# Kernel optimization log

Hardware: AMD Instinct MI355X
Metric: run time of the kernel (lower is better)

Reference implementation:

```python
import jax, jax.numpy as jnp
import numpy as np

T, H, NH, NKV, HD = 2048, 1024, 16, 4, 64
I, E, TOPK = 2048, 8, 2
EPS = 1e-5
ROPE_BASE = 10000.0


def rms_norm(x, w):
    var = jnp.mean(x * x, axis=-1, keepdims=True)
    return x * jax.lax.rsqrt(var + EPS) * w


def apply_rope(x, positions, n_heads):
    # neox-style rotary over full head_dim
    t = x.reshape(-1, n_heads, HD)
    half = HD // 2
    inv_freq = 1.0 / (ROPE_BASE ** (jnp.arange(0, half, dtype=jnp.float32) / half))
    freqs = positions.astype(jnp.float32)[:, None] * inv_freq[None, :]  # [T, half]
    cos = jnp.cos(freqs)[:, None, :]
    sin = jnp.sin(freqs)[:, None, :]
    x1, x2 = t[..., :half], t[..., half:]
    rot = jnp.concatenate([x1 * cos - x2 * sin, x2 * cos + x1 * sin], axis=-1)
    return rot.reshape(x.shape)


def setup_inputs():
    key = jax.random.key(0)
    ks = jax.random.split(key, 9)
    s = 0.02
    return dict(
        positions=jnp.arange(T, dtype=jnp.int32),
        hidden_states=jax.random.normal(ks[0], (T, H), jnp.float32),
        input_ln_w=jnp.ones((H,), jnp.float32),
        post_ln_w=jnp.ones((H,), jnp.float32),
        residual_ln_w=jnp.ones((H,), jnp.float32),
        qkv_w=jax.random.normal(ks[1], ((NH + 2 * NKV) * HD, H), jnp.float32) * s,
        o_w=jax.random.normal(ks[2], (H, NH * HD), jnp.float32) * s,
        gate_w=jax.random.normal(ks[3], (E, H), jnp.float32) * s,
        ws=jax.random.normal(ks[4], (E, 2 * I, H), jnp.float32) * s,
        w2s=jax.random.normal(ks[5], (E, H, I), jnp.float32) * s,
        res_w13=jax.random.normal(ks[6], (2 * H, H), jnp.float32) * s,
        res_w2=jax.random.normal(ks[7], (H, H), jnp.float32) * s,
    )


def attention(x, positions, qkv_w, o_w):
    qkv = x @ qkv_w.T  # [T, (NH+2*NKV)*HD]
    q, k, v = jnp.split(qkv, [NH * HD, NH * HD + NKV * HD], axis=-1)
    q = apply_rope(q, positions, NH)
    k = apply_rope(k, positions, NKV)
    q = q.reshape(T, NH, HD)
    k = k.reshape(T, NKV, HD)
    v = v.reshape(T, NKV, HD)
    rep = NH // NKV  # GQA: repeat kv heads
    k = jnp.repeat(k, rep, axis=1)
    v = jnp.repeat(v, rep, axis=1)
    scale = HD ** -0.5
    scores = jnp.einsum('tnd,snd->nts', q, k) * scale  # [NH, T, T]
    causal = jnp.tril(jnp.ones((T, T), dtype=bool))
    scores = jnp.where(causal[None], scores, -jnp.inf)
    probs = jax.nn.softmax(scores, axis=-1)
    out = jnp.einsum('nts,snd->tnd', probs, v).reshape(T, NH * HD)
    return out @ o_w.T


def silu_and_mul(gu):
    g, u = jnp.split(gu, 2, axis=-1)
    return jax.nn.silu(g) * u


def moe(x, gate_w, ws, w2s):
    logits = x @ gate_w.T  # [T, E]
    probs = jax.nn.softmax(logits, axis=-1)
    topk_w, topk_ids = jax.lax.top_k(probs, TOPK)
    topk_w = topk_w / jnp.sum(topk_w, axis=-1, keepdims=True)  # renormalize (top_k > 1)
    routes = jnp.zeros((x.shape[0], E), x.dtype).at[
        jnp.arange(x.shape[0])[:, None], topk_ids].set(topk_w)  # [T, E] sparse routing
    gu = jnp.einsum('th,eih->tei', x, ws)        # [T, E, 2I]
    act = silu_and_mul(gu)                        # [T, E, I]
    eo = jnp.einsum('tei,ehi->teh', act, w2s)     # [T, E, H]
    return jnp.einsum('te,teh->th', routes, eo)


def reference(positions, hidden_states, input_ln_w, post_ln_w, residual_ln_w,
              qkv_w, o_w, gate_w, ws, w2s, res_w13, res_w2):
    residual_input = hidden_states
    h = rms_norm(hidden_states, input_ln_w)
    h = attention(h, positions, qkv_w, o_w)
    residual_attn = residual_input + h
    # parallel residual MLP branch (ffn_dim == hidden)
    r = rms_norm(residual_attn, residual_ln_w)
    r = silu_and_mul(r @ res_w13.T) @ res_w2.T
    residual_mlp = residual_attn + r
    # MoE branch
    m = rms_norm(residual_attn, post_ln_w)
    m = moe(m, gate_w, ws, w2s)
    return residual_mlp + m
```

## Files before the change

kernel.cpp:

```cpp
#include <hip/hip_runtime.h>
#include <stdint.h>


typedef _Float16 f16;
typedef _Float16 f16x8 __attribute__((ext_vector_type(8)));
typedef _Float16 f16x4 __attribute__((ext_vector_type(4)));
typedef float f32x4 __attribute__((ext_vector_type(4)));

#define DEV __device__ __forceinline__

DEV void glds16(const void* g, void* l) {
  __builtin_amdgcn_global_load_lds((const __attribute__((address_space(1))) void*)g,
                                   (__attribute__((address_space(3))) void*)l, 16, 0, 0);
}

__global__ void cvt_f16_kernel(const float* __restrict__ in, f16* __restrict__ outp) {
  const size_t i = ((size_t)blockIdx.x * 256 + threadIdx.x) * 4;
  float4 f = *(const float4*)(in + i);
  f16x4 o;
  o[0] = (f16)f.x; o[1] = (f16)f.y; o[2] = (f16)f.z; o[3] = (f16)f.w;
  *(f16x4*)(outp + i) = o;
}

__global__ void cvt_f16x2_kernel(const float* __restrict__ in,
                                 f16* __restrict__ oh, f16* __restrict__ ol) {
  const size_t i = ((size_t)blockIdx.x * 256 + threadIdx.x) * 4;
  float4 f = *(const float4*)(in + i);
  f16x4 h, l;
  h[0] = (f16)f.x; l[0] = (f16)(f.x - (float)h[0]);
  h[1] = (f16)f.y; l[1] = (f16)(f.y - (float)h[1]);
  h[2] = (f16)f.z; l[2] = (f16)(f.z - (float)h[2]);
  h[3] = (f16)f.w; l[3] = (f16)(f.w - (float)h[3]);
  *(f16x4*)(oh + i) = h;
  *(f16x4*)(ol + i) = l;
}

__global__ void rmsnorm_kernel(const float* __restrict__ in, const float* __restrict__ w,
                               f16* __restrict__ outp) {
  const int t = blockIdx.x * 4 + (threadIdx.x >> 6);
  const int lane = threadIdx.x & 63;
  const float* x = in + (size_t)t * 1024;
  float v[16]; float ss = 0.f;
#pragma unroll
  for (int j = 0; j < 16; j++) { float a = x[lane + 64 * j]; v[j] = a; ss += a * a; }
#pragma unroll
  for (int m = 1; m < 64; m <<= 1) ss += __shfl_xor(ss, m);
  const float rs = rsqrtf(ss * (1.f / 1024.f) + 1e-5f);
#pragma unroll
  for (int j = 0; j < 16; j++)
    outp[(size_t)t * 1024 + lane + 64 * j] = (f16)(v[j] * rs * w[lane + 64 * j]);
}

__global__ void rmsnorm_dual_kernel(const float* __restrict__ in,
                                    const float* __restrict__ w1, const float* __restrict__ w2,
                                    f16* __restrict__ o1, f16* __restrict__ o2) {
  const int t = blockIdx.x * 4 + (threadIdx.x >> 6);
  const int lane = threadIdx.x & 63;
  const float* x = in + (size_t)t * 1024;
  float v[16]; float ss = 0.f;
#pragma unroll
  for (int j = 0; j < 16; j++) { float a = x[lane + 64 * j]; v[j] = a; ss += a * a; }
#pragma unroll
  for (int m = 1; m < 64; m <<= 1) ss += __shfl_xor(ss, m);
  const float rs = rsqrtf(ss * (1.f / 1024.f) + 1e-5f);
#pragma unroll
  for (int j = 0; j < 16; j++) {
    float nv = v[j] * rs;
    size_t idx = (size_t)t * 1024 + lane + 64 * j;
    o1[idx] = (f16)(nv * w1[lane + 64 * j]);
    o2[idx] = (f16)(nv * w2[lane + 64 * j]);
  }
}

template <int EPI, int BN>
__global__ __launch_bounds__(256) void gemm_f16_kernel(
    const f16* __restrict__ A, const f16* __restrict__ B,
    void* __restrict__ outp, const float* __restrict__ addsrc,
    int M, int N, int K) {
  constexpr int JT = BN / 32;
  __shared__ __attribute__((aligned(16))) f16 As[128 * 32];
  __shared__ __attribute__((aligned(16))) f16 Bs[BN * 32];
  const int tid = threadIdx.x;
  const size_t row0 = (size_t)blockIdx.y * 128, col0 = (size_t)blockIdx.x * BN;
  const int c0 = tid, c1 = tid + 256;
  const f16* a0 = A + (row0 + (c0 >> 2)) * K + (c0 & 3) * 8;
  const f16* a1 = A + (row0 + (c1 >> 2)) * K + (c1 & 3) * 8;
  const f16* b0 = B + (col0 + (c0 >> 2)) * K + (c0 & 3) * 8;
  const f16* b1 = B + (col0 + ((BN == 128) ? (c1 >> 2) : 0)) * K + (c1 & 3) * 8;

  const int wave = tid >> 6, lane = tid & 63, lr = lane >> 4, lc = lane & 15;
  const int wr = wave >> 1, wc = wave & 1;

  f32x4 acc[4][JT];
#pragma unroll
  for (int i = 0; i < 4; i++)
#pragma unroll
    for (int j = 0; j < JT; j++) acc[i][j] = (f32x4){0.f, 0.f, 0.f, 0.f};

  for (int k0 = 0; k0 < K; k0 += 32) {
    glds16(a0 + k0, As + c0 * 8); glds16(a1 + k0, As + c1 * 8);
    glds16(b0 + k0, Bs + c0 * 8);
    if constexpr (BN == 128) glds16(b1 + k0, Bs + c1 * 8);
    __syncthreads();
    f16x8 af[4], bfr[JT];
#pragma unroll
    for (int i = 0; i < 4; i++)
      af[i] = *(const f16x8*)(As + (wr * 64 + i * 16 + lc) * 32 + lr * 8);
#pragma unroll
    for (int j = 0; j < JT; j++)
      bfr[j] = *(const f16x8*)(Bs + (wc * (BN / 2) + j * 16 + lc) * 32 + lr * 8);
#pragma unroll
    for (int i = 0; i < 4; i++)
#pragma unroll
      for (int j = 0; j < JT; j++)
        acc[i][j] = __builtin_amdgcn_mfma_f32_16x16x32_f16(af[i], bfr[j], acc[i][j], 0, 0, 0);
    __syncthreads();
  }

#pragma unroll
  for (int i = 0; i < 4; i++)
#pragma unroll
    for (int j = 0; j < JT; j++) {
      const size_t rbase = row0 + wr * 64 + i * 16 + lr * 4;
      const size_t col = col0 + wc * (BN / 2) + j * 16 + lc;
#pragma unroll
      for (int r = 0; r < 4; r++) {
        size_t idx = (rbase + r) * N + col;
        if constexpr (EPI == 0) ((float*)outp)[idx] = acc[i][j][r];
        else if constexpr (EPI == 1) ((float*)outp)[idx] = acc[i][j][r] + addsrc[idx];
        else ((f16*)outp)[idx] = (f16)acc[i][j][r];
      }
    }
}

__global__ __launch_bounds__(256) void gemm_f16x2_add_kernel(
    const f16* __restrict__ Ah, const f16* __restrict__ Al,
    const f16* __restrict__ Bh, const f16* __restrict__ Bl,
    float* __restrict__ outp, const float* __restrict__ addsrc,
    int M, int N, int K) {
  __shared__ __attribute__((aligned(16))) f16 Ash[128 * 32];
  __shared__ __attribute__((aligned(16))) f16 Asl[128 * 32];
  __shared__ __attribute__((aligned(16))) f16 Bsh[64 * 32];
  __shared__ __attribute__((aligned(16))) f16 Bsl[64 * 32];
  const int tid = threadIdx.x;
  const size_t row0 = (size_t)blockIdx.y * 128, col0 = (size_t)blockIdx.x * 64;
  const int c0 = tid, c1 = tid + 256;
  const size_t aoff0 = (row0 + (c0 >> 2)) * K + (c0 & 3) * 8;
  const size_t aoff1 = (row0 + (c1 >> 2)) * K + (c1 & 3) * 8;
  const size_t boff0 = (col0 + (c0 >> 2)) * K + (c0 & 3) * 8;

  const int wave = tid >> 6, lane = tid & 63, lr = lane >> 4, lc = lane & 15;
  const int wr = wave >> 1, wc = wave & 1;

  f32x4 acc[4][2];
#pragma unroll
  for (int i = 0; i < 4; i++)
#pragma unroll
    for (int j = 0; j < 2; j++) acc[i][j] = (f32x4){0.f, 0.f, 0.f, 0.f};

  for (int k0 = 0; k0 < K; k0 += 32) {
    glds16(Ah + aoff0 + k0, Ash + c0 * 8); glds16(Ah + aoff1 + k0, Ash + c1 * 8);
    glds16(Al + aoff0 + k0, Asl + c0 * 8); glds16(Al + aoff1 + k0, Asl + c1 * 8);
    glds16(Bh + boff0 + k0, Bsh + c0 * 8);
    glds16(Bl + boff0 + k0, Bsl + c0 * 8);
    __syncthreads();
    f16x8 afh[4], afl[4], bfh[2], bfl[2];
#pragma unroll
    for (int i = 0; i < 4; i++) {
      const int ro = (wr * 64 + i * 16 + lc) * 32 + lr * 8;
      afh[i] = *(const f16x8*)(Ash + ro);
      afl[i] = *(const f16x8*)(Asl + ro);
    }
#pragma unroll
    for (int j = 0; j < 2; j++) {
      const int ro = (wc * 32 + j * 16 + lc) * 32 + lr * 8;
      bfh[j] = *(const f16x8*)(Bsh + ro);
      bfl[j] = *(const f16x8*)(Bsl + ro);
    }
#pragma unroll
    for (int i = 0; i < 4; i++)
#pragma unroll
      for (int j = 0; j < 2; j++) {
        acc[i][j] = __builtin_amdgcn_mfma_f32_16x16x32_f16(afh[i], bfh[j], acc[i][j], 0, 0, 0);
        acc[i][j] = __builtin_amdgcn_mfma_f32_16x16x32_f16(afh[i], bfl[j], acc[i][j], 0, 0, 0);
        acc[i][j] = __builtin_amdgcn_mfma_f32_16x16x32_f16(afl[i], bfh[j], acc[i][j], 0, 0, 0);
      }
    __syncthreads();
  }

#pragma unroll
  for (int i = 0; i < 4; i++)
#pragma unroll
    for (int j = 0; j < 2; j++) {
      const size_t rbase = row0 + wr * 64 + i * 16 + lr * 4;
      const size_t col = col0 + wc * 32 + j * 16 + lc;
#pragma unroll
      for (int r = 0; r < 4; r++) {
        size_t idx = (rbase + r) * N + col;
        outp[idx] = acc[i][j][r] + addsrc[idx];
      }
    }
}

template <int DIVROW, int BN>
__global__ __launch_bounds__(256) void gemm_moe_kernel(
    const f16* __restrict__ A, const f16* __restrict__ Ball, f16* __restrict__ outp,
    const int* __restrict__ perm, const int* __restrict__ counts,
    int N, int K, size_t strideB) {
  constexpr int JT = BN / 32;
  const int e = blockIdx.z;
  const int cnt = counts[e];
  const int bm = blockIdx.y;
  if (bm * 128 >= cnt) return;
  const f16* B = Ball + (size_t)e * strideB;
  __shared__ __attribute__((aligned(16))) f16 As[128 * 32];
  __shared__ __attribute__((aligned(16))) f16 Bs[BN * 32];
  const int tid = threadIdx.x;
  const size_t col0 = (size_t)blockIdx.x * BN;
  const int c0 = tid, c1 = tid + 256;
  const int pbase = e * 2048 + bm * 128;
  const int rt0 = c0 >> 2, rt1 = c1 >> 2;
  const int sid0 = (bm * 128 + rt0 < cnt) ? perm[pbase + rt0] : -1;
  const int sid1 = (bm * 128 + rt1 < cnt) ? perm[pbase + rt1] : -1;
  const size_t ar0 = DIVROW ? (size_t)(sid0 >> 1) : (size_t)sid0;
  const size_t ar1 = DIVROW ? (size_t)(sid1 >> 1) : (size_t)sid1;
  const f16* ap0 = A + ar0 * K + (c0 & 3) * 8;
  const f16* ap1 = A + ar1 * K + (c1 & 3) * 8;
  const f16* b0 = B + (col0 + (c0 >> 2)) * K + (c0 & 3) * 8;
  const f16* b1 = B + (col0 + ((BN == 128) ? (c1 >> 2) : 0)) * K + (c1 & 3) * 8;

  const int wave = tid >> 6, lane = tid & 63, lr = lane >> 4, lc = lane & 15;
  const int wr = wave >> 1, wc = wave & 1;

  f32x4 acc[4][JT];
#pragma unroll
  for (int i = 0; i < 4; i++)
#pragma unroll
    for (int j = 0; j < JT; j++) acc[i][j] = (f32x4){0.f, 0.f, 0.f, 0.f};

  for (int k0 = 0; k0 < K; k0 += 32) {
    glds16(b0 + k0, Bs + c0 * 8);
    if constexpr (BN == 128) glds16(b1 + k0, Bs + c1 * 8);
    f16x8 va0, va1;
#pragma unroll
    for (int x = 0; x < 8; x++) { va0[x] = (f16)0.f; va1[x] = (f16)0.f; }
    if (sid0 >= 0) va0 = *(const f16x8*)(ap0 + k0);
    if (sid1 >= 0) va1 = *(const f16x8*)(ap1 + k0);
    *(f16x8*)(As + c0 * 8) = va0;
    *(f16x8*)(As + c1 * 8) = va1;
    __syncthreads();
    f16x8 af[4], bfr[JT];
#pragma unroll
    for (int i = 0; i < 4; i++)
      af[i] = *(const f16x8*)(As + (wr * 64 + i * 16 + lc) * 32 + lr * 8);
#pragma unroll
    for (int j = 0; j < JT; j++)
      bfr[j] = *(const f16x8*)(Bs + (wc * (BN / 2) + j * 16 + lc) * 32 + lr * 8);
#pragma unroll
    for (int i = 0; i < 4; i++)
#pragma unroll
      for (int j = 0; j < JT; j++)
        acc[i][j] = __builtin_amdgcn_mfma_f32_16x16x32_f16(af[i], bfr[j], acc[i][j], 0, 0, 0);
    __syncthreads();
  }

  int sids[4][4];
#pragma unroll
  for (int i = 0; i < 4; i++)
#pragma unroll
    for (int r = 0; r < 4; r++) {
      int rit = wr * 64 + i * 16 + lr * 4 + r;
      sids[i][r] = (bm * 128 + rit < cnt) ? perm[pbase + rit] : -1;
    }
#pragma unroll
  for (int i = 0; i < 4; i++)
#pragma unroll
    for (int j = 0; j < JT; j++) {
      const size_t col = col0 + wc * (BN / 2) + j * 16 + lc;
#pragma unroll
      for (int r = 0; r < 4; r++)
        if (sids[i][r] >= 0)
          outp[(size_t)sids[i][r] * N + col] = (f16)acc[i][j][r];
    }
}

__global__ void rope_kernel(const float* __restrict__ qkv, const int* __restrict__ pos,
                            f16* __restrict__ qr, f16* __restrict__ kr) {
  const int t = blockIdx.y;
  const int u = blockIdx.x * 256 + threadIdx.x;
  if (u >= 640) return;
  const float* base = qkv + (size_t)t * 1536;
  const int head = u >> 5, i = u & 31;
  const bool isq = head < 16;
  const int off = isq ? head * 64 + i : 1024 + (head - 16) * 64 + i;
  const float x1 = base[off], x2 = base[off + 32];
  const double ph = (double)pos[t] * exp((double)i * -0.28782313662425575);
  const float c = (float)cos(ph), s = (float)sin(ph);
  const float r1 = x1 * c - x2 * s, r2 = x2 * c + x1 * s;
  if (isq) {
    const float qs = 0.18033688011116042f;
    qr[(size_t)t * 1024 + head * 64 + i] = (f16)(qs * r1);
    qr[(size_t)t * 1024 + head * 64 + i + 32] = (f16)(qs * r2);
  } else {
    const int kh = head - 16;
    kr[(size_t)t * 256 + kh * 64 + i] = (f16)r1;
    kr[(size_t)t * 256 + kh * 64 + i + 32] = (f16)r2;
  }
}

__global__ void vtrans_kernel(const float* __restrict__ qkvf, f16* __restrict__ vt) {
  __shared__ float Ts[64 * 69];
  const int t0 = blockIdx.x * 64;
  const int kv = blockIdx.y;
  const int tid = threadIdx.x;
  const int tr = tid >> 2, jj = tid & 3;
  const float* src = qkvf + (size_t)(t0 + tr) * 1536 + 1280 + kv * 64 + jj * 16;
#pragma unroll
  for (int x = 0; x < 4; x++) {
    float4 f = *(const float4*)(src + x * 4);
    Ts[tr * 69 + jj * 16 + x * 4 + 0] = f.x;
    Ts[tr * 69 + jj * 16 + x * 4 + 1] = f.y;
    Ts[tr * 69 + jj * 16 + x * 4 + 2] = f.z;
    Ts[tr * 69 + jj * 16 + x * 4 + 3] = f.w;
  }
  __syncthreads();
  f16* dst = vt + (size_t)(kv * 64 + tr) * 2048 + t0 + jj * 16;
#pragma unroll
  for (int x = 0; x < 2; x++) {
    f16x8 o;
#pragma unroll
    for (int i = 0; i < 8; i++) o[i] = (f16)Ts[(jj * 16 + x * 8 + i) * 69 + tr];
    *(f16x8*)(dst + x * 8) = o;
  }
}

__global__ __launch_bounds__(256, 3) void attn_kernel(
    const f16* __restrict__ qr, const f16* __restrict__ kr, const f16* __restrict__ vt,
    f16* __restrict__ ahi, f16* __restrict__ alo) {
  const int qt = 31 - (int)blockIdx.x;
  const int h = blockIdx.y;
  const int kvh = h >> 2;
  __shared__ __attribute__((aligned(16))) f16 Ks[128 * 72];
  __shared__ __attribute__((aligned(16))) f16 Vs[64 * 136];
  __shared__ __attribute__((aligned(16))) f16 Pl[4 * 16 * 136];
  const int tid = threadIdx.x;
  const int wave = tid >> 6, lane = tid & 63, lr = lane >> 4, lc = lane & 15;
  const int trow = qt * 64 + wave * 16 + lc;
  f16* Pw = Pl + wave * 16 * 136;

  const int krow = tid >> 3, kcol = (tid & 7) * 8;
  const int vrow = tid >> 4, vcol = (tid & 15) * 8;
  const f16* kgbase = kr + (size_t)kvh * 64 + kcol;
  const f16* vgbase = vt + (size_t)(kvh * 64 + vrow) * 2048 + vcol;

  const f16* qp = qr + (size_t)trow * 1024 + h * 64 + lr * 8;
  f16x8 qf0 = *(const f16x8*)(qp);
  f16x8 qf1 = *(const f16x8*)(qp + 32);

  float m_run = -3e38f, l_run = 0.f;
  f32x4 accO[4];
#pragma unroll
  for (int jo = 0; jo < 4; jo++) accO[jo] = (f32x4){0.f, 0.f, 0.f, 0.f};

  const int nch = (qt >> 1) + 1;

  f16x8 kreg[4], vreg[4];
#pragma unroll
  for (int it = 0; it < 4; it++) {
    kreg[it] = *(const f16x8*)(kgbase + (size_t)(it * 32 + krow) * 256);
    vreg[it] = *(const f16x8*)(vgbase + it * 16 * 2048);
  }

  for (int ch = 0; ch < nch; ++ch) {
    const int c0 = ch * 128;
    const bool last = (ch == nch - 1);

    __syncthreads();
#pragma unroll
    for (int it = 0; it < 4; it++) {
      *(f16x8*)(Ks + (it * 32 + krow) * 72 + kcol) = kreg[it];
      *(f16x8*)(Vs + (it * 16 + vrow) * 136 + vcol) = vreg[it];
    }
    __syncthreads();

    if (!last) {
      const int c1 = c0 + 128;
#pragma unroll
      for (int it = 0; it < 4; it++) {
        kreg[it] = *(const f16x8*)(kgbase + (size_t)(c1 + it * 32 + krow) * 256);
        vreg[it] = *(const f16x8*)(vgbase + it * 16 * 2048 + c1);
      }
    }

    f32x4 st[8];
#pragma unroll
    for (int j = 0; j < 8; j++) {
      const f16* kp = Ks + (j * 16 + lc) * 72 + lr * 8;
      f16x8 ka0 = *(const f16x8*)(kp);
      f16x8 ka1 = *(const f16x8*)(kp + 32);
      f32x4 s = (f32x4){0.f, 0.f, 0.f, 0.f};
      s = __builtin_amdgcn_mfma_f32_16x16x32_f16(ka0, qf0, s, 0, 0, 0);
      s = __builtin_amdgcn_mfma_f32_16x16x32_f16(ka1, qf1, s, 0, 0, 0);
      st[j] = s;
    }

    if (last) {
#pragma unroll
      for (int j = 0; j < 8; j++)
#pragma unroll
        for (int r = 0; r < 4; r++)
          if (c0 + j * 16 + lr * 4 + r > trow) st[j][r] = -3e38f;
    }

    float mc = -3e38f;
#pragma unroll
    for (int j = 0; j < 8; j++)
      mc = fmaxf(mc, fmaxf(fmaxf(st[j][0], st[j][1]), fmaxf(st[j][2], st[j][3])));
    mc = fmaxf(mc, __shfl_xor(mc, 16));
    mc = fmaxf(mc, __shfl_xor(mc, 32));
    const float mn = fmaxf(m_run, mc);
    const float alpha = __builtin_amdgcn_exp2f(m_run - mn);
    m_run = mn;

    float ls = 0.f;
#pragma unroll
    for (int j = 0; j < 8; j++) {
      f16x4 pv;
#pragma unroll
      for (int r = 0; r < 4; r++) {
        float e = __builtin_amdgcn_exp2f(st[j][r] - mn);
        ls += e;
        pv[r] = (f16)e;
      }
      *(f16x4*)(Pw + lc * 136 + j * 16 + lr * 4) = pv;
    }
    ls += __shfl_xor(ls, 16);
    ls += __shfl_xor(ls, 32);
    l_run = l_run * alpha + ls;
#pragma unroll
    for (int jo = 0; jo < 4; jo++) accO[jo] *= alpha;

#pragma unroll
    for (int kkt = 0; kkt < 4; kkt++) {
      f16x8 pb = *(const f16x8*)(Pw + lc * 136 + kkt * 32 + lr * 8);
#pragma unroll
      for (int jo = 0; jo < 4; jo++) {
        f16x8 va = *(const f16x8*)(Vs + (jo * 16 + lc) * 136 + kkt * 32 + lr * 8);
        accO[jo] = __builtin_amdgcn_mfma_f32_16x16x32_f16(va, pb, accO[jo], 0, 0, 0);
      }
    }
  }

  const float inv = 1.f / l_run;
#pragma unroll
  for (int jo = 0; jo < 4; jo++) {
    f16x4 hi4, lo4;
#pragma unroll
    for (int r = 0; r < 4; r++) {
      float o = accO[jo][r] * inv;
      f16 hv = (f16)o;
      hi4[r] = hv;
      lo4[r] = (f16)(o - (float)hv);
    }
    const size_t idx = (size_t)trow * 1024 + h * 64 + jo * 16 + lr * 4;
    *(f16x4*)(ahi + idx) = hi4;
    *(f16x4*)(alo + idx) = lo4;
  }
}

__global__ void routing_kernel(const float* __restrict__ resA,
                               const float* __restrict__ postw,
                               const float* __restrict__ gw,
                               int* __restrict__ counts, int* __restrict__ perm,
                               float* __restrict__ rw) {
  const int t = blockIdx.x * 4 + (threadIdx.x >> 6);
  const int lane = threadIdx.x & 63;
  const float* x = resA + (size_t)t * 1024;
  float v[16]; float ss = 0.f;
#pragma unroll
  for (int j = 0; j < 16; j++) { float a = x[lane + 64 * j]; v[j] = a; ss += a * a; }
#pragma unroll
  for (int m = 1; m < 64; m <<= 1) ss += __shfl_xor(ss, m);
  const float rs = rsqrtf(ss * (1.f / 1024.f) + 1e-5f);
#pragma unroll
  for (int j = 0; j < 16; j++) v[j] *= rs * postw[lane + 64 * j];
  float lg[8];
#pragma unroll
  for (int e = 0; e < 8; e++) {
    float p = 0.f;
    const float* g = gw + (size_t)e * 1024;
#pragma unroll
    for (int j = 0; j < 16; j++) p += v[j] * g[lane + 64 * j];
#pragma unroll
    for (int m = 1; m < 64; m <<= 1) p += __shfl_xor(p, m);
    lg[e] = p;
  }
  if (lane == 0) {
    int e0 = 0; float b0 = lg[0];
#pragma unroll
    for (int e = 1; e < 8; e++) if (lg[e] > b0) { b0 = lg[e]; e0 = e; }
    int e1 = -1; float b1 = -3e38f;
#pragma unroll
    for (int e = 0; e < 8; e++) if (e != e0 && lg[e] > b1) { b1 = lg[e]; e1 = e; }
    const float w0 = 1.f / (1.f + expf(b1 - b0));
    const float w1 = 1.f - w0;
    int p0 = atomicAdd(&counts[e0], 1);
    perm[e0 * 2048 + p0] = t * 2;
    int p1 = atomicAdd(&counts[e1], 1);
    perm[e1 * 2048 + p1] = t * 2 + 1;
    rw[t * 2] = w0;
    rw[t * 2 + 1] = w1;
  }
}

__global__ void silu_mul_kernel(const f16* __restrict__ gu, f16* __restrict__ outp, int lgN) {
  const int N = 1 << lgN;
  const size_t i4 = ((size_t)blockIdx.x * 256 + threadIdx.x) * 4;
  const size_t r = i4 >> lgN;
  const int c = (int)(i4 & (N - 1));
  const f16* gp = gu + r * (size_t)(2 * N) + c;
  f16x4 g = *(const f16x4*)gp;
  f16x4 u = *(const f16x4*)(gp + N);
  f16x4 o;
#pragma unroll
  for (int x = 0; x < 4; x++) {
    float gg = (float)g[x], uu = (float)u[x];
    o[x] = (f16)(gg / (1.f + __expf(-gg)) * uu);
  }
  *(f16x4*)(outp + r * (size_t)N + c) = o;
}

__global__ void final_add_kernel(float* __restrict__ outp, const f16* __restrict__ eo,
                                 const float* __restrict__ rw) {
  const size_t i4 = ((size_t)blockIdx.x * 256 + threadIdx.x) * 4;
  const int t = (int)(i4 >> 10);
  const int c = (int)(i4 & 1023);
  const float w0 = rw[2 * t], w1 = rw[2 * t + 1];
  f16x4 a = *(const f16x4*)(eo + ((size_t)(2 * t)) * 1024 + c);
  f16x4 b = *(const f16x4*)(eo + ((size_t)(2 * t + 1)) * 1024 + c);
  float4 o = *(float4*)(outp + i4);
  o.x += w0 * (float)a[0] + w1 * (float)b[0];
  o.y += w0 * (float)a[1] + w1 * (float)b[1];
  o.z += w0 * (float)a[2] + w1 * (float)b[2];
  o.w += w0 * (float)a[3] + w1 * (float)b[3];
  *(float4*)(outp + i4) = o;
}

extern "C" void kernel_launch(void* const* d_in, const int* in_sizes, int n_in,
                              void* d_out, int out_size, void* d_ws, size_t ws_size,
                              hipStream_t stream) {
  const int* positions = (const int*)d_in[0];
  const float* hidden = (const float*)d_in[1];
  const float* in_ln = (const float*)d_in[2];
  const float* post_ln = (const float*)d_in[3];
  const float* res_ln = (const float*)d_in[4];
  const float* qkv_w = (const float*)d_in[5];
  const float* o_w = (const float*)d_in[6];
  const float* gate_w = (const float*)d_in[7];
  const float* ws_w = (const float*)d_in[8];
  const float* w2s_w = (const float*)d_in[9];
  const float* w13_w = (const float*)d_in[10];
  const float* w2_w = (const float*)d_in[11];
  float* out = (float*)d_out;

  char* p = (char*)d_ws;
  auto alloc = [&](size_t b) { void* r = (void*)p; p += (b + 255) & ~(size_t)255; return r; };

  f16* wqkv = (f16*)alloc((size_t)1536 * 1024 * 2);
  f16* woh  = (f16*)alloc((size_t)1024 * 1024 * 2);
  f16* wol  = (f16*)alloc((size_t)1024 * 1024 * 2);
  f16* wws  = (f16*)alloc((size_t)8 * 4096 * 1024 * 2);
  f16* ww2  = (f16*)alloc((size_t)8 * 1024 * 2048 * 2);
  f16* w13  = (f16*)alloc((size_t)2048 * 1024 * 2);
  f16* w2c  = (f16*)alloc((size_t)1024 * 1024 * 2);
  f16* hn   = (f16*)alloc((size_t)2048 * 1024 * 2);
  float* qkvf = (float*)alloc((size_t)2048 * 1536 * 4);
  f16* qr = (f16*)alloc((size_t)2048 * 1024 * 2);
  f16* kr = (f16*)alloc((size_t)2048 * 256 * 2);
  f16* vt = (f16*)alloc((size_t)256 * 2048 * 2);
  f16* ath = (f16*)alloc((size_t)2048 * 1024 * 2);
  f16* atl = (f16*)alloc((size_t)2048 * 1024 * 2);
  float* resA = (float*)alloc((size_t)2048 * 1024 * 4);
  f16* rn = (f16*)alloc((size_t)2048 * 1024 * 2);
  f16* mn = (f16*)alloc((size_t)2048 * 1024 * 2);
  f16* gu13 = (f16*)alloc((size_t)2048 * 2048 * 2);
  f16* act13 = (f16*)alloc((size_t)2048 * 1024 * 2);
  f16* gum = (f16*)alloc((size_t)4096 * 4096 * 2);
  f16* actm = (f16*)alloc((size_t)4096 * 2048 * 2);
  f16* eo = (f16*)alloc((size_t)4096 * 1024 * 2);
  float* rw = (float*)alloc((size_t)4096 * 4);
  int* counts = (int*)alloc(256);
  int* perm = (int*)alloc((size_t)8 * 2048 * 4);

  cvt_f16_kernel<<<dim3(1536 * 1024 / 1024), dim3(256), 0, stream>>>(qkv_w, wqkv);
  cvt_f16_kernel<<<dim3(8 * 4096 * 1024 / 1024), dim3(256), 0, stream>>>(ws_w, wws);
  cvt_f16_kernel<<<dim3(8 * 1024 * 2048 / 1024), dim3(256), 0, stream>>>(w2s_w, ww2);
  cvt_f16_kernel<<<dim3(2048 * 1024 / 1024), dim3(256), 0, stream>>>(w13_w, w13);
  cvt_f16_kernel<<<dim3(1024 * 1024 / 1024), dim3(256), 0, stream>>>(w2_w, w2c);
  cvt_f16x2_kernel<<<dim3(1024 * 1024 / 1024), dim3(256), 0, stream>>>(o_w, woh, wol);
  hipMemsetAsync(counts, 0, 256, stream);

  rmsnorm_kernel<<<dim3(512), dim3(256), 0, stream>>>(hidden, in_ln, hn);
  gemm_f16_kernel<0, 64><<<dim3(24, 16), dim3(256), 0, stream>>>(
      hn, wqkv, (void*)qkvf, (const float*)nullptr, 2048, 1536, 1024);
  rope_kernel<<<dim3(3, 2048), dim3(256), 0, stream>>>(qkvf, positions, qr, kr);
  vtrans_kernel<<<dim3(32, 4), dim3(256), 0, stream>>>(qkvf, vt);
  attn_kernel<<<dim3(32, 16), dim3(256), 0, stream>>>(qr, kr, vt, ath, atl);
  gemm_f16x2_add_kernel<<<dim3(16, 16), dim3(256), 0, stream>>>(
      ath, atl, woh, wol, resA, hidden, 2048, 1024, 1024);

  rmsnorm_dual_kernel<<<dim3(512), dim3(256), 0, stream>>>(resA, res_ln, post_ln, rn, mn);
  routing_kernel<<<dim3(512), dim3(256), 0, stream>>>(resA, post_ln, gate_w, counts, perm, rw);

  gemm_f16_kernel<2, 64><<<dim3(32, 16), dim3(256), 0, stream>>>(
      rn, w13, (void*)gu13, (const float*)nullptr, 2048, 2048, 1024);
  silu_mul_kernel<<<dim3(2048 * 1024 / 1024), dim3(256), 0, stream>>>(gu13, act13, 10);
  gemm_f16_kernel<1, 64><<<dim3(16, 16), dim3(256), 0, stream>>>(
      act13, w2c, (void*)out, resA, 2048, 1024, 1024);

  gemm_moe_kernel<1, 128><<<dim3(32, 16, 8), dim3(256), 0, stream>>>(
      mn, wws, gum, perm, counts, 4096, 1024, (size_t)4096 * 1024);
  silu_mul_kernel<<<dim3(4096 * 2048 / 1024), dim3(256), 0, stream>>>(gum, actm, 11);
  gemm_moe_kernel<0, 64><<<dim3(16, 16, 8), dim3(256), 0, stream>>>(
      actm, ww2, eo, perm, counts, 1024, 2048, (size_t)1024 * 2048);
  final_add_kernel<<<dim3(2048 * 1024 / 1024), dim3(256), 0, stream>>>(out, eo, rw);
}
```

Before: 668.7 us.

## Double-buffer LDS tiles in GEMM kernels to overlap loads with MFMA

Adds two-stage LDS double buffering to the dense, split-f16 and MoE GEMM kernels. The next K-tile is prefetched into the alternate buffer while MFMAs run on the current one, and one barrier per iteration is dropped. It also widens the MoE down-projection tile from BN=64 to BN=128. The cost is double the LDS per block, which may lower occupancy, and more registers in the MoE kernel.

```diff
diff --git a/kernel.cpp b/kernel.cpp
--- a/kernel.cpp
+++ b/kernel.cpp
@@ -78,8 +78,8 @@
     void* __restrict__ outp, const float* __restrict__ addsrc,
     int M, int N, int K) {
   constexpr int JT = BN / 32;
-  __shared__ __attribute__((aligned(16))) f16 As[128 * 32];
-  __shared__ __attribute__((aligned(16))) f16 Bs[BN * 32];
+  __shared__ __attribute__((aligned(16))) f16 As[2][128 * 32];
+  __shared__ __attribute__((aligned(16))) f16 Bs[2][BN * 32];
   const int tid = threadIdx.x;
   const size_t row0 = (size_t)blockIdx.y * 128, col0 = (size_t)blockIdx.x * BN;
   const int c0 = tid, c1 = tid + 256;
@@ -97,24 +97,32 @@
 #pragma unroll
     for (int j = 0; j < JT; j++) acc[i][j] = (f32x4){0.f, 0.f, 0.f, 0.f};
 
+  auto stage = [&](int k0, int buf) {
+    glds16(a0 + k0, As[buf] + c0 * 8);
+    glds16(a1 + k0, As[buf] + c1 * 8);
+    glds16(b0 + k0, Bs[buf] + c0 * 8);
+    if constexpr (BN == 128) glds16(b1 + k0, Bs[buf] + c1 * 8);
+  };
+
+  stage(0, 0);
+  __syncthreads();
+  int cur = 0;
   for (int k0 = 0; k0 < K; k0 += 32) {
-    glds16(a0 + k0, As + c0 * 8); glds16(a1 + k0, As + c1 * 8);
-    glds16(b0 + k0, Bs + c0 * 8);
-    if constexpr (BN == 128) glds16(b1 + k0, Bs + c1 * 8);
-    __syncthreads();
+    if (k0 + 32 < K) stage(k0 + 32, cur ^ 1);
     f16x8 af[4], bfr[JT];
 #pragma unroll
     for (int i = 0; i < 4; i++)
-      af[i] = *(const f16x8*)(As + (wr * 64 + i * 16 + lc) * 32 + lr * 8);
+      af[i] = *(const f16x8*)(As[cur] + (wr * 64 + i * 16 + lc) * 32 + lr * 8);
 #pragma unroll
     for (int j = 0; j < JT; j++)
-      bfr[j] = *(const f16x8*)(Bs + (wc * (BN / 2) + j * 16 + lc) * 32 + lr * 8);
+      bfr[j] = *(const f16x8*)(Bs[cur] + (wc * (BN / 2) + j * 16 + lc) * 32 + lr * 8);
 #pragma unroll
     for (int i = 0; i < 4; i++)
 #pragma unroll
       for (int j = 0; j < JT; j++)
         acc[i][j] = __builtin_amdgcn_mfma_f32_16x16x32_f16(af[i], bfr[j], acc[i][j], 0, 0, 0);
     __syncthreads();
+    cur ^= 1;
   }
 
 #pragma unroll
@@ -138,10 +146,10 @@
     const f16* __restrict__ Bh, const f16* __restrict__ Bl,
     float* __restrict__ outp, const float* __restrict__ addsrc,
     int M, int N, int K) {
-  __shared__ __attribute__((aligned(16))) f16 Ash[128 * 32];
-  __shared__ __attribute__((aligned(16))) f16 Asl[128 * 32];
-  __shared__ __attribute__((aligned(16))) f16 Bsh[64 * 32];
-  __shared__ __attribute__((aligned(16))) f16 Bsl[64 * 32];
+  __shared__ __attribute__((aligned(16))) f16 Ash[2][128 * 32];
+  __shared__ __attribute__((aligned(16))) f16 Asl[2][128 * 32];
+  __shared__ __attribute__((aligned(16))) f16 Bsh[2][64 * 32];
+  __shared__ __attribute__((aligned(16))) f16 Bsl[2][64 * 32];
   const int tid = threadIdx.x;
   const size_t row0 = (size_t)blockIdx.y * 128, col0 = (size_t)blockIdx.x * 64;
   const int c0 = tid, c1 = tid + 256;
@@ -158,24 +166,32 @@
 #pragma unroll
     for (int j = 0; j < 2; j++) acc[i][j] = (f32x4){0.f, 0.f, 0.f, 0.f};
 
+  auto stage = [&](int k0, int buf) {
+    glds16(Ah + aoff0 + k0, Ash[buf] + c0 * 8);
+    glds16(Ah + aoff1 + k0, Ash[buf] + c1 * 8);
+    glds16(Al + aoff0 + k0, Asl[buf] + c0 * 8);
+    glds16(Al + aoff1 + k0, Asl[buf] + c1 * 8);
+    glds16(Bh + boff0 + k0, Bsh[buf] + c0 * 8);
+    glds16(Bl + boff0 + k0, Bsl[buf] + c0 * 8);
+  };
+
+  stage(0, 0);
+  __syncthreads();
+  int cur = 0;
   for (int k0 = 0; k0 < K; k0 += 32) {
-    glds16(Ah + aoff0 + k0, Ash + c0 * 8); glds16(Ah + aoff1 + k0, Ash + c1 * 8);
-    glds16(Al + aoff0 + k0, Asl + c0 * 8); glds16(Al + aoff1 + k0, Asl + c1 * 8);
-    glds16(Bh + boff0 + k0, Bsh + c0 * 8);
-    glds16(Bl + boff0 + k0, Bsl + c0 * 8);
-    __syncthreads();
+    if (k0 + 32 < K) stage(k0 + 32, cur ^ 1);
     f16x8 afh[4], afl[4], bfh[2], bfl[2];
 #pragma unroll
     for (int i = 0; i < 4; i++) {
       const int ro = (wr * 64 + i * 16 + lc) * 32 + lr * 8;
-      afh[i] = *(const f16x8*)(Ash + ro);
-      afl[i] = *(const f16x8*)(Asl + ro);
+      afh[i] = *(const f16x8*)(Ash[cur] + ro);
+      afl[i] = *(const f16x8*)(Asl[cur] + ro);
     }
 #pragma unroll
     for (int j = 0; j < 2; j++) {
       const int ro = (wc * 32 + j * 16 + lc) * 32 + lr * 8;
-      bfh[j] = *(const f16x8*)(Bsh + ro);
-      bfl[j] = *(const f16x8*)(Bsl + ro);
+      bfh[j] = *(const f16x8*)(Bsh[cur] + ro);
+      bfl[j] = *(const f16x8*)(Bsl[cur] + ro);
     }
 #pragma unroll
     for (int i = 0; i < 4; i++)
@@ -186,6 +202,7 @@
         acc[i][j] = __builtin_amdgcn_mfma_f32_16x16x32_f16(afl[i], bfh[j], acc[i][j], 0, 0, 0);
       }
     __syncthreads();
+    cur ^= 1;
   }
 
 #pragma unroll
@@ -213,8 +230,8 @@
   const int bm = blockIdx.y;
   if (bm * 128 >= cnt) return;
   const f16* B = Ball + (size_t)e * strideB;
-  __shared__ __attribute__((aligned(16))) f16 As[128 * 32];
-  __shared__ __attribute__((aligned(16))) f16 Bs[BN * 32];
+  __shared__ __attribute__((aligned(16))) f16 As[2][128 * 32];
+  __shared__ __attribute__((aligned(16))) f16 Bs[2][BN * 32];
   const int tid = threadIdx.x;
   const size_t col0 = (size_t)blockIdx.x * BN;
   const int c0 = tid, c1 = tid + 256;
@@ -238,30 +255,45 @@
 #pragma unroll
     for (int j = 0; j < JT; j++) acc[i][j] = (f32x4){0.f, 0.f, 0.f, 0.f};
 
-  for (int k0 = 0; k0 < K; k0 += 32) {
-    glds16(b0 + k0, Bs + c0 * 8);
-    if constexpr (BN == 128) glds16(b1 + k0, Bs + c1 * 8);
-    f16x8 va0, va1;
+  auto stageB = [&](int k0, int buf) {
+    glds16(b0 + k0, Bs[buf] + c0 * 8);
+    if constexpr (BN == 128) glds16(b1 + k0, Bs[buf] + c1 * 8);
+  };
+  auto loadA = [&](int k0, f16x8& va0, f16x8& va1) {
 #pragma unroll
     for (int x = 0; x < 8; x++) { va0[x] = (f16)0.f; va1[x] = (f16)0.f; }
     if (sid0 >= 0) va0 = *(const f16x8*)(ap0 + k0);
     if (sid1 >= 0) va1 = *(const f16x8*)(ap1 + k0);
-    *(f16x8*)(As + c0 * 8) = va0;
-    *(f16x8*)(As + c1 * 8) = va1;
-    __syncthreads();
+  };
+
+  f16x8 va0, va1;
+  loadA(0, va0, va1);
+  stageB(0, 0);
+  *(f16x8*)(As[0] + c0 * 8) = va0;
+  *(f16x8*)(As[0] + c1 * 8) = va1;
+  __syncthreads();
+  int cur = 0;
+  for (int k0 = 0; k0 < K; k0 += 32) {
+    const bool nxt = (k0 + 32 < K);
+    if (nxt) { stageB(k0 + 32, cur ^ 1); loadA(k0 + 32, va0, va1); }
     f16x8 af[4], bfr[JT];
 #pragma unroll
     for (int i = 0; i < 4; i++)
-      af[i] = *(const f16x8*)(As + (wr * 64 + i * 16 + lc) * 32 + lr * 8);
+      af[i] = *(const f16x8*)(As[cur] + (wr * 64 + i * 16 + lc) * 32 + lr * 8);
 #pragma unroll
     for (int j = 0; j < JT; j++)
-      bfr[j] = *(const f16x8*)(Bs + (wc * (BN / 2) + j * 16 + lc) * 32 + lr * 8);
+      bfr[j] = *(const f16x8*)(Bs[cur] + (wc * (BN / 2) + j * 16 + lc) * 32 + lr * 8);
 #pragma unroll
     for (int i = 0; i < 4; i++)
 #pragma unroll
       for (int j = 0; j < JT; j++)
         acc[i][j] = __builtin_amdgcn_mfma_f32_16x16x32_f16(af[i], bfr[j], acc[i][j], 0, 0, 0);
+    if (nxt) {
+      *(f16x8*)(As[cur ^ 1] + c0 * 8) = va0;
+      *(f16x8*)(As[cur ^ 1] + c1 * 8) = va1;
+    }
     __syncthreads();
+    cur ^= 1;
   }
 
   int sids[4][4];
@@ -621,7 +653,7 @@
   gemm_moe_kernel<1, 128><<<dim3(32, 16, 8), dim3(256), 0, stream>>>(
       mn, wws, gum, perm, counts, 4096, 1024, (size_t)4096 * 1024);
   silu_mul_kernel<<<dim3(4096 * 2048 / 1024), dim3(256), 0, stream>>>(gum, actm, 11);
-  gemm_moe_kernel<0, 64><<<dim3(16, 16, 8), dim3(256), 0, stream>>>(
+  gemm_moe_kernel<0, 128><<<dim3(8, 16, 8), dim3(256), 0, stream>>>(
       actm, ww2, eo, perm, counts, 1024, 2048, (size_t)1024 * 2048);
   final_add_kernel<<<dim3(2048 * 1024 / 1024), dim3(256), 0, stream>>>(out, eo, rw);
 }
```

Result: no change. 661.1 us (-1.1%).
